# Kernel optimization log

Measured on AMD Instinct MI355X. Metric: run time of the kernel, lower is better.

## Reference

```python
import jax, jax.numpy as jnp
import numpy as np

N_NODES = 100000
N_EDGES = 1600000
IN_FEAT = 128
N_HEADS = 8
OUT_FEAT = 16


def setup_inputs() -> dict:
    key = jax.random.key(0)
    k1, k2, k3, k4, k5 = jax.random.split(key, 5)
    x = jax.random.normal(k1, (N_NODES, IN_FEAT), dtype=jnp.float32)
    edge_index = jax.random.randint(k2, (2, N_EDGES), 0, N_NODES)
    # Glorot-uniform params as in init_params
    lim_w = float(np.sqrt(6.0 / (IN_FEAT + N_HEADS * OUT_FEAT)))
    W = jax.random.uniform(k3, (IN_FEAT, N_HEADS * OUT_FEAT), minval=-lim_w, maxval=lim_w, dtype=jnp.float32)
    lim_a = float(np.sqrt(6.0 / (1 + N_HEADS * OUT_FEAT)))
    a_src = jax.random.uniform(k4, (N_HEADS, OUT_FEAT), minval=-lim_a, maxval=lim_a, dtype=jnp.float32)
    a_tgt = jax.random.uniform(k5, (N_HEADS, OUT_FEAT), minval=-lim_a, maxval=lim_a, dtype=jnp.float32)
    bias = jnp.zeros((OUT_FEAT,), dtype=jnp.float32)
    return {"in_nodes_features": x, "edge_index": edge_index, "W": W, "a_src": a_src, "a_tgt": a_tgt, "bias": bias}


def reference(in_nodes_features, edge_index, W, a_src, a_tgt, bias):
    # Single GATLayerImp3 with concat=False, activation=Softmax (GAT, num_of_layers=2).
    # Dropout disabled (eval / dropout=0.0).
    N = in_nodes_features.shape[0]
    H, F = a_src.shape
    proj = (in_nodes_features @ W).reshape(N, H, F)            # [N, H, F]
    s_src = jnp.einsum('nhf,hf->nh', proj, a_src)              # [N, H]
    s_tgt = jnp.einsum('nhf,hf->nh', proj, a_tgt)              # [N, H]
    src, tgt = edge_index[0], edge_index[1]
    # lift + per-edge LeakyReLU(0.2) scoring
    e = jax.nn.leaky_relu(s_src[src] + s_tgt[tgt], negative_slope=0.2)  # [E, H]
    # numerically stable segment softmax over edges sharing a target node
    seg_max = jax.ops.segment_max(e, tgt, num_segments=N)      # [N, H]
    seg_max = jnp.where(jnp.isfinite(seg_max), seg_max, 0.0)
    ex = jnp.exp(e - seg_max[tgt])                             # [E, H]
    denom = jax.ops.segment_sum(ex, tgt, num_segments=N)       # [N, H]
    alpha = ex / (denom[tgt] + 1e-16)                          # [E, H]
    # weighted message + scatter-add aggregation
    msg = proj[src] * alpha[:, :, None]                        # [E, H, F]
    out = jax.ops.segment_sum(msg, tgt, num_segments=N)        # [N, H, F]
    out = out.mean(axis=1) + bias                              # concat=False -> mean over heads
    return jax.nn.softmax(out, axis=-1)                        # final-layer Softmax activation
```

## Files before the change

### kernel.cpp

```cpp
#include <hip/hip_runtime.h>

#define NN 100000
#define NE 1600000

static __device__ __forceinline__ unsigned short f32_to_bf16_rne(float x) {
    unsigned int u = __float_as_uint(x);
    u += 0x7fff + ((u >> 16) & 1);
    return (unsigned short)(u >> 16);
}
static __device__ __forceinline__ float bf16_to_f32(unsigned int bits16) {
    return __uint_as_float(bits16 << 16);
}

__global__ __launch_bounds__(256) void gemm_score_kernel(const float* __restrict__ x,
                                                         const float* __restrict__ W,
                                                         const float* __restrict__ a_src,
                                                         const float* __restrict__ a_tgt,
                                                         unsigned short* __restrict__ projT,
                                                         unsigned short* __restrict__ s_src_b,
                                                         unsigned short* __restrict__ s_tgt_b) {
    __shared__ float sXT[32][68];
    __shared__ float sW[32][128];
    const int t = threadIdx.x;
    const int n0 = blockIdx.x * 64;
    const int c0 = (t & 31) * 4;
    const int r0 = t >> 5;
    float acc[8][4];
#pragma unroll
    for (int i = 0; i < 8; i++)
#pragma unroll
        for (int j = 0; j < 4; j++) acc[i][j] = 0.f;

    for (int kt = 0; kt < 128; kt += 32) {
#pragma unroll
        for (int p = 0; p < 2; p++) {
            int idx = t + p * 256;
            int r = idx >> 3;
            int kk = idx & 7;
            float4 v = make_float4(0.f, 0.f, 0.f, 0.f);
            int n = n0 + r;
            if (n < NN) v = *reinterpret_cast<const float4*>(&x[(size_t)n * 128 + kt + kk * 4]);
            sXT[kk * 4 + 0][r] = v.x;
            sXT[kk * 4 + 1][r] = v.y;
            sXT[kk * 4 + 2][r] = v.z;
            sXT[kk * 4 + 3][r] = v.w;
        }
#pragma unroll
        for (int p = 0; p < 4; p++) {
            int idx = t + p * 256;
            int kr = idx >> 5;
            int c4 = idx & 31;
            float4 v = *reinterpret_cast<const float4*>(&W[(size_t)(kt + kr) * 128 + c4 * 4]);
            *reinterpret_cast<float4*>(&sW[kr][c4 * 4]) = v;
        }
        __syncthreads();
#pragma unroll
        for (int k = 0; k < 32; k++) {
            float4 xa = *reinterpret_cast<const float4*>(&sXT[k][r0 * 8]);
            float4 xb = *reinterpret_cast<const float4*>(&sXT[k][r0 * 8 + 4]);
            float4 wv = *reinterpret_cast<const float4*>(&sW[k][c0]);
            float xs[8] = {xa.x, xa.y, xa.z, xa.w, xb.x, xb.y, xb.z, xb.w};
#pragma unroll
            for (int i = 0; i < 8; i++) {
                acc[i][0] += xs[i] * wv.x;
                acc[i][1] += xs[i] * wv.y;
                acc[i][2] += xs[i] * wv.z;
                acc[i][3] += xs[i] * wv.w;
            }
        }
        __syncthreads();
    }
    const int h  = c0 >> 4;
    const int f0 = c0 & 15;
    const float aS0 = a_src[c0], aS1 = a_src[c0 + 1], aS2 = a_src[c0 + 2], aS3 = a_src[c0 + 3];
    const float aT0 = a_tgt[c0], aT1 = a_tgt[c0 + 1], aT2 = a_tgt[c0 + 2], aT3 = a_tgt[c0 + 3];
#pragma unroll
    for (int i = 0; i < 8; i++) {
        int n = n0 + r0 * 8 + i;
        if (n < NN) {
            unsigned short* pT = &projT[(size_t)n * 128];
#pragma unroll
            for (int j = 0; j < 4; j++) pT[(f0 + j) * 8 + h] = f32_to_bf16_rne(acc[i][j]);
            float ss = acc[i][0] * aS0 + acc[i][1] * aS1 + acc[i][2] * aS2 + acc[i][3] * aS3;
            float st = acc[i][0] * aT0 + acc[i][1] * aT1 + acc[i][2] * aT2 + acc[i][3] * aT3;
            ss += __shfl_xor(ss, 1);
            ss += __shfl_xor(ss, 2);
            st += __shfl_xor(st, 1);
            st += __shfl_xor(st, 2);
            if ((t & 3) == 0) {
                s_src_b[(size_t)n * 8 + h] = f32_to_bf16_rne(ss);
                s_tgt_b[(size_t)n * 8 + h] = f32_to_bf16_rne(st);
            }
        }
    }
}

__global__ __launch_bounds__(256) void denom_kernel(const int* __restrict__ src,
                                                    const int* __restrict__ tgt,
                                                    const unsigned short* __restrict__ s_src_b,
                                                    const unsigned short* __restrict__ s_tgt_b,
                                                    float* __restrict__ denom,
                                                    unsigned short* __restrict__ exb) {
    int gid = blockIdx.x * blockDim.x + threadIdx.x;
    int e = gid >> 3;
    if (e >= NE) return;
    int h = gid & 7;
    int s = src[e], t = tgt[e];
    float v = bf16_to_f32(s_src_b[(size_t)s * 8 + h]) + bf16_to_f32(s_tgt_b[(size_t)t * 8 + h]);
    v = v >= 0.f ? v : 0.2f * v;
    float ex = expf(v);
    exb[(size_t)e * 8 + h] = f32_to_bf16_rne(ex);
    atomicAdd(&denom[(size_t)t * 8 + h], ex);
}

__global__ __launch_bounds__(256) void aggregate_kernel(const int* __restrict__ src,
                                                        const int* __restrict__ tgt,
                                                        const float* __restrict__ denom,
                                                        const unsigned short* __restrict__ exb,
                                                        const unsigned short* __restrict__ projT,
                                                        float* __restrict__ out_acc) {
    int gid = blockIdx.x * blockDim.x + threadIdx.x;
    int e = gid >> 4;
    int lane = gid & 15;
    if (e >= NE) return;
    int s = src[e], t = tgt[e];
    int h = lane & 7;
    float ex = bf16_to_f32(exb[(size_t)e * 8 + h]);
    float alpha = ex / (denom[(size_t)t * 8 + h] + 1e-16f);
    uint4 v = *reinterpret_cast<const uint4*>(&projT[(size_t)s * 128 + lane * 8]);
    float p0 = bf16_to_f32(v.x & 0xffffu), p1 = bf16_to_f32(v.x >> 16);
    float p2 = bf16_to_f32(v.y & 0xffffu), p3 = bf16_to_f32(v.y >> 16);
    float p4 = bf16_to_f32(v.z & 0xffffu), p5 = bf16_to_f32(v.z >> 16);
    float p6 = bf16_to_f32(v.w & 0xffffu), p7 = bf16_to_f32(v.w >> 16);
    float m = 0.f;
    m += __shfl(alpha, 0, 16) * p0;
    m += __shfl(alpha, 1, 16) * p1;
    m += __shfl(alpha, 2, 16) * p2;
    m += __shfl(alpha, 3, 16) * p3;
    m += __shfl(alpha, 4, 16) * p4;
    m += __shfl(alpha, 5, 16) * p5;
    m += __shfl(alpha, 6, 16) * p6;
    m += __shfl(alpha, 7, 16) * p7;
    atomicAdd(&out_acc[(size_t)t * 16 + lane], m * 0.125f);
}

__global__ __launch_bounds__(256) void softmax_kernel(const float* __restrict__ out_acc,
                                                      const float* __restrict__ bias,
                                                      float* __restrict__ out) {
    int gid = blockIdx.x * blockDim.x + threadIdx.x;
    int n = gid >> 4;
    int lane = gid & 15;
    if (n >= NN) return;
    float v = out_acc[(size_t)n * 16 + lane] + bias[lane];
    float mx = v;
#pragma unroll
    for (int m = 1; m < 16; m <<= 1) mx = fmaxf(mx, __shfl_xor(mx, m, 64));
    float ex = expf(v - mx);
    float sum = ex;
#pragma unroll
    for (int m = 1; m < 16; m <<= 1) sum += __shfl_xor(sum, m, 64);
    out[(size_t)n * 16 + lane] = ex / sum;
}

extern "C" void kernel_launch(void* const* d_in, const int* in_sizes, int n_in,
                              void* d_out, int out_size, void* d_ws, size_t ws_size,
                              hipStream_t stream) {
    const float* x     = (const float*)d_in[0];
    const int*   ei    = (const int*)d_in[1];
    const float* W     = (const float*)d_in[2];
    const float* a_src = (const float*)d_in[3];
    const float* a_tgt = (const float*)d_in[4];
    const float* bias  = (const float*)d_in[5];
    float* out = (float*)d_out;

    const int* src = ei;
    const int* tgt = ei + NE;

    char* ws = (char*)d_ws;
    size_t off = 0;
    auto alloc = [&](size_t bytes) {
        char* p = ws + off;
        off += (bytes + 255) & ~(size_t)255;
        return p;
    };
    unsigned short* projT   = (unsigned short*)alloc((size_t)NN * 128 * 2);
    unsigned short* exb     = (unsigned short*)alloc((size_t)NE * 8 * 2);
    unsigned short* s_src_b = (unsigned short*)alloc((size_t)NN * 8 * 2);
    unsigned short* s_tgt_b = (unsigned short*)alloc((size_t)NN * 8 * 2);
    float*          denom   = (float*)alloc((size_t)NN * 8 * 4);
    float*          out_acc = (float*)alloc((size_t)NN * 16 * 4);

    hipMemsetAsync(denom, 0, (size_t)NN * 8 * 4, stream);
    hipMemsetAsync(out_acc, 0, (size_t)NN * 16 * 4, stream);

    gemm_score_kernel<<<(NN + 63) / 64, 256, 0, stream>>>(x, W, a_src, a_tgt, projT, s_src_b, s_tgt_b);
    denom_kernel<<<((size_t)NE * 8 + 255) / 256, 256, 0, stream>>>(src, tgt, s_src_b, s_tgt_b, denom, exb);
    aggregate_kernel<<<((size_t)NE * 16 + 255) / 256, 256, 0, stream>>>(src, tgt, denom, exb,
                                                                        projT, out_acc);
    softmax_kernel<<<(NN * 16 + 255) / 256, 256, 0, stream>>>(out_acc, bias, out);
}
```

Measured before the change: 247.7 us.

## Recompute edge exponentials in aggregate instead of storing them; enlarge GEMM tile

The denom kernel no longer writes per-edge exp values to a bf16 buffer. The aggregate kernel recomputes them from the per-node source and target scores, which removes a 25.6 MB write and its later read in exchange for extra score gathers and exp work per edge. The projection GEMM now processes 128 nodes per block with a row-major shared tile and 16 accumulators per thread instead of 64 nodes with a transposed tile. That raises register use and changes the shared-memory access pattern.

After: 289.0 us. 1.17x slower.

```diff
diff --git a/kernel.cpp b/kernel.cpp
--- a/kernel.cpp
+++ b/kernel.cpp
@@ -19,31 +19,28 @@
                                                          unsigned short* __restrict__ projT,
                                                          unsigned short* __restrict__ s_src_b,
                                                          unsigned short* __restrict__ s_tgt_b) {
-    __shared__ float sXT[32][68];
+    __shared__ float sX[128][32];
     __shared__ float sW[32][128];
     const int t = threadIdx.x;
-    const int n0 = blockIdx.x * 64;
+    const int n0 = blockIdx.x * 128;
     const int c0 = (t & 31) * 4;
     const int r0 = t >> 5;
-    float acc[8][4];
+    float acc[16][4];
 #pragma unroll
-    for (int i = 0; i < 8; i++)
+    for (int i = 0; i < 16; i++)
 #pragma unroll
         for (int j = 0; j < 4; j++) acc[i][j] = 0.f;
 
     for (int kt = 0; kt < 128; kt += 32) {
 #pragma unroll
-        for (int p = 0; p < 2; p++) {
+        for (int p = 0; p < 4; p++) {
             int idx = t + p * 256;
             int r = idx >> 3;
             int kk = idx & 7;
             float4 v = make_float4(0.f, 0.f, 0.f, 0.f);
             int n = n0 + r;
             if (n < NN) v = *reinterpret_cast<const float4*>(&x[(size_t)n * 128 + kt + kk * 4]);
-            sXT[kk * 4 + 0][r] = v.x;
-            sXT[kk * 4 + 1][r] = v.y;
-            sXT[kk * 4 + 2][r] = v.z;
-            sXT[kk * 4 + 3][r] = v.w;
+            *reinterpret_cast<float4*>(&sX[r][kk * 4]) = v;
         }
 #pragma unroll
         for (int p = 0; p < 4; p++) {
@@ -56,16 +53,14 @@
         __syncthreads();
 #pragma unroll
         for (int k = 0; k < 32; k++) {
-            float4 xa = *reinterpret_cast<const float4*>(&sXT[k][r0 * 8]);
-            float4 xb = *reinterpret_cast<const float4*>(&sXT[k][r0 * 8 + 4]);
             float4 wv = *reinterpret_cast<const float4*>(&sW[k][c0]);
-            float xs[8] = {xa.x, xa.y, xa.z, xa.w, xb.x, xb.y, xb.z, xb.w};
 #pragma unroll
-            for (int i = 0; i < 8; i++) {
-                acc[i][0] += xs[i] * wv.x;
-                acc[i][1] += xs[i] * wv.y;
-                acc[i][2] += xs[i] * wv.z;
-                acc[i][3] += xs[i] * wv.w;
+            for (int i = 0; i < 16; i++) {
+                float xv = sX[r0 + 8 * i][k];
+                acc[i][0] += xv * wv.x;
+                acc[i][1] += xv * wv.y;
+                acc[i][2] += xv * wv.z;
+                acc[i][3] += xv * wv.w;
             }
         }
         __syncthreads();
@@ -75,8 +70,8 @@
     const float aS0 = a_src[c0], aS1 = a_src[c0 + 1], aS2 = a_src[c0 + 2], aS3 = a_src[c0 + 3];
     const float aT0 = a_tgt[c0], aT1 = a_tgt[c0 + 1], aT2 = a_tgt[c0 + 2], aT3 = a_tgt[c0 + 3];
 #pragma unroll
-    for (int i = 0; i < 8; i++) {
-        int n = n0 + r0 * 8 + i;
+    for (int i = 0; i < 16; i++) {
+        int n = n0 + r0 + 8 * i;
         if (n < NN) {
             unsigned short* pT = &projT[(size_t)n * 128];
 #pragma unroll
@@ -99,8 +94,7 @@
                                                     const int* __restrict__ tgt,
                                                     const unsigned short* __restrict__ s_src_b,
                                                     const unsigned short* __restrict__ s_tgt_b,
-                                                    float* __restrict__ denom,
-                                                    unsigned short* __restrict__ exb) {
+                                                    float* __restrict__ denom) {
     int gid = blockIdx.x * blockDim.x + threadIdx.x;
     int e = gid >> 3;
     if (e >= NE) return;
@@ -108,15 +102,14 @@
     int s = src[e], t = tgt[e];
     float v = bf16_to_f32(s_src_b[(size_t)s * 8 + h]) + bf16_to_f32(s_tgt_b[(size_t)t * 8 + h]);
     v = v >= 0.f ? v : 0.2f * v;
-    float ex = expf(v);
-    exb[(size_t)e * 8 + h] = f32_to_bf16_rne(ex);
-    atomicAdd(&denom[(size_t)t * 8 + h], ex);
+    atomicAdd(&denom[(size_t)t * 8 + h], expf(v));
 }
 
 __global__ __launch_bounds__(256) void aggregate_kernel(const int* __restrict__ src,
                                                         const int* __restrict__ tgt,
+                                                        const unsigned short* __restrict__ s_src_b,
+                                                        const unsigned short* __restrict__ s_tgt_b,
                                                         const float* __restrict__ denom,
-                                                        const unsigned short* __restrict__ exb,
                                                         const unsigned short* __restrict__ projT,
                                                         float* __restrict__ out_acc) {
     int gid = blockIdx.x * blockDim.x + threadIdx.x;
@@ -125,7 +118,9 @@
     if (e >= NE) return;
     int s = src[e], t = tgt[e];
     int h = lane & 7;
-    float ex = bf16_to_f32(exb[(size_t)e * 8 + h]);
+    float v0 = bf16_to_f32(s_src_b[(size_t)s * 8 + h]) + bf16_to_f32(s_tgt_b[(size_t)t * 8 + h]);
+    v0 = v0 >= 0.f ? v0 : 0.2f * v0;
+    float ex = expf(v0);
     float alpha = ex / (denom[(size_t)t * 8 + h] + 1e-16f);
     uint4 v = *reinterpret_cast<const uint4*>(&projT[(size_t)s * 128 + lane * 8]);
     float p0 = bf16_to_f32(v.x & 0xffffu), p1 = bf16_to_f32(v.x >> 16);
@@ -184,7 +179,6 @@
         return p;
     };
     unsigned short* projT   = (unsigned short*)alloc((size_t)NN * 128 * 2);
-    unsigned short* exb     = (unsigned short*)alloc((size_t)NE * 8 * 2);
     unsigned short* s_src_b = (unsigned short*)alloc((size_t)NN * 8 * 2);
     unsigned short* s_tgt_b = (unsigned short*)alloc((size_t)NN * 8 * 2);
     float*          denom   = (float*)alloc((size_t)NN * 8 * 4);
@@ -193,9 +187,9 @@
     hipMemsetAsync(denom, 0, (size_t)NN * 8 * 4, stream);
     hipMemsetAsync(out_acc, 0, (size_t)NN * 16 * 4, stream);
 
-    gemm_score_kernel<<<(NN + 63) / 64, 256, 0, stream>>>(x, W, a_src, a_tgt, projT, s_src_b, s_tgt_b);
-    denom_kernel<<<((size_t)NE * 8 + 255) / 256, 256, 0, stream>>>(src, tgt, s_src_b, s_tgt_b, denom, exb);
-    aggregate_kernel<<<((size_t)NE * 16 + 255) / 256, 256, 0, stream>>>(src, tgt, denom, exb,
-                                                                        projT, out_acc);
+    gemm_score_kernel<<<(NN + 127) / 128, 256, 0, stream>>>(x, W, a_src, a_tgt, projT, s_src_b, s_tgt_b);
+    denom_kernel<<<((size_t)NE * 8 + 255) / 256, 256, 0, stream>>>(src, tgt, s_src_b, s_tgt_b, denom);
+    aggregate_kernel<<<((size_t)NE * 16 + 255) / 256, 256, 0, stream>>>(src, tgt, s_src_b, s_tgt_b,
+                                                                        denom, projT, out_acc);
     softmax_kernel<<<(NN * 16 + 255) / 256, 256, 0, stream>>>(out_acc, bias, out);
 }
```

## Bucket edges by target block and fuse softmax-aggregate into per-bucket kernel

Applied to the files above, without the earlier changes.

Edges are counting-sorted into buckets of 128 target nodes, using a histogram, a scan and a scatter that packs src and local target into one int. A single fused kernel per bucket then computes the edge softmax denominators, the weighted aggregation and the final softmax in shared memory. This replaces global atomics, the exb buffer and two memsets. It adds three sorting kernels and shared-memory atomics, and the fused kernel may suffer from uneven bucket sizes and only 782 blocks.

New measurement: 440.6 us. 1.78x slower.

```diff
diff --git a/kernel.cpp b/kernel.cpp
--- a/kernel.cpp
+++ b/kernel.cpp
@@ -2,6 +2,7 @@
 
 #define NN 100000
 #define NE 1600000
+#define NBUCK 782
 
 static __device__ __forceinline__ unsigned short f32_to_bf16_rne(float x) {
     unsigned int u = __float_as_uint(x);
@@ -95,71 +96,146 @@
     }
 }
 
-__global__ __launch_bounds__(256) void denom_kernel(const int* __restrict__ src,
-                                                    const int* __restrict__ tgt,
-                                                    const unsigned short* __restrict__ s_src_b,
-                                                    const unsigned short* __restrict__ s_tgt_b,
-                                                    float* __restrict__ denom,
-                                                    unsigned short* __restrict__ exb) {
-    int gid = blockIdx.x * blockDim.x + threadIdx.x;
-    int e = gid >> 3;
-    if (e >= NE) return;
-    int h = gid & 7;
-    int s = src[e], t = tgt[e];
-    float v = bf16_to_f32(s_src_b[(size_t)s * 8 + h]) + bf16_to_f32(s_tgt_b[(size_t)t * 8 + h]);
-    v = v >= 0.f ? v : 0.2f * v;
-    float ex = expf(v);
-    exb[(size_t)e * 8 + h] = f32_to_bf16_rne(ex);
-    atomicAdd(&denom[(size_t)t * 8 + h], ex);
-}
-
-__global__ __launch_bounds__(256) void aggregate_kernel(const int* __restrict__ src,
-                                                        const int* __restrict__ tgt,
-                                                        const float* __restrict__ denom,
-                                                        const unsigned short* __restrict__ exb,
-                                                        const unsigned short* __restrict__ projT,
-                                                        float* __restrict__ out_acc) {
-    int gid = blockIdx.x * blockDim.x + threadIdx.x;
-    int e = gid >> 4;
-    int lane = gid & 15;
-    if (e >= NE) return;
-    int s = src[e], t = tgt[e];
-    int h = lane & 7;
-    float ex = bf16_to_f32(exb[(size_t)e * 8 + h]);
-    float alpha = ex / (denom[(size_t)t * 8 + h] + 1e-16f);
-    uint4 v = *reinterpret_cast<const uint4*>(&projT[(size_t)s * 128 + lane * 8]);
-    float p0 = bf16_to_f32(v.x & 0xffffu), p1 = bf16_to_f32(v.x >> 16);
-    float p2 = bf16_to_f32(v.y & 0xffffu), p3 = bf16_to_f32(v.y >> 16);
-    float p4 = bf16_to_f32(v.z & 0xffffu), p5 = bf16_to_f32(v.z >> 16);
-    float p6 = bf16_to_f32(v.w & 0xffffu), p7 = bf16_to_f32(v.w >> 16);
-    float m = 0.f;
-    m += __shfl(alpha, 0, 16) * p0;
-    m += __shfl(alpha, 1, 16) * p1;
-    m += __shfl(alpha, 2, 16) * p2;
-    m += __shfl(alpha, 3, 16) * p3;
-    m += __shfl(alpha, 4, 16) * p4;
-    m += __shfl(alpha, 5, 16) * p5;
-    m += __shfl(alpha, 6, 16) * p6;
-    m += __shfl(alpha, 7, 16) * p7;
-    atomicAdd(&out_acc[(size_t)t * 16 + lane], m * 0.125f);
-}
-
-__global__ __launch_bounds__(256) void softmax_kernel(const float* __restrict__ out_acc,
-                                                      const float* __restrict__ bias,
-                                                      float* __restrict__ out) {
-    int gid = blockIdx.x * blockDim.x + threadIdx.x;
-    int n = gid >> 4;
-    int lane = gid & 15;
-    if (n >= NN) return;
-    float v = out_acc[(size_t)n * 16 + lane] + bias[lane];
-    float mx = v;
-#pragma unroll
-    for (int m = 1; m < 16; m <<= 1) mx = fmaxf(mx, __shfl_xor(mx, m, 64));
-    float ex = expf(v - mx);
-    float sum = ex;
-#pragma unroll
-    for (int m = 1; m < 16; m <<= 1) sum += __shfl_xor(sum, m, 64);
-    out[(size_t)n * 16 + lane] = ex / sum;
+__global__ __launch_bounds__(256) void bucket_hist_kernel(const int* __restrict__ tgt,
+                                                          int* __restrict__ counts) {
+    __shared__ int bins[NBUCK];
+    for (int i = threadIdx.x; i < NBUCK; i += 256) bins[i] = 0;
+    __syncthreads();
+    int base = blockIdx.x * 2048;
+#pragma unroll
+    for (int i = 0; i < 8; i++) {
+        int e = base + i * 256 + threadIdx.x;
+        if (e < NE) atomicAdd(&bins[tgt[e] >> 7], 1);
+    }
+    __syncthreads();
+    for (int i = threadIdx.x; i < NBUCK; i += 256)
+        if (bins[i]) atomicAdd(&counts[i], bins[i]);
+}
+
+__global__ __launch_bounds__(1024) void bucket_scan_kernel(const int* __restrict__ counts,
+                                                           int* __restrict__ base,
+                                                           int* __restrict__ gcursor) {
+    __shared__ int sc[1024];
+    int t = threadIdx.x;
+    int v = (t < NBUCK) ? counts[t] : 0;
+    sc[t] = v;
+    __syncthreads();
+    for (int off = 1; off < 1024; off <<= 1) {
+        int u = (t >= off) ? sc[t - off] : 0;
+        __syncthreads();
+        sc[t] += u;
+        __syncthreads();
+    }
+    if (t < NBUCK) {
+        int ex = sc[t] - v;
+        base[t] = ex;
+        gcursor[t] = ex;
+    }
+    if (t == NBUCK - 1) base[NBUCK] = sc[t];
+}
+
+__global__ __launch_bounds__(256) void bucket_scatter_kernel(const int* __restrict__ src,
+                                                             const int* __restrict__ tgt,
+                                                             int* __restrict__ gcursor,
+                                                             int* __restrict__ sorted) {
+    __shared__ int bins[NBUCK];
+    __shared__ int basel[NBUCK];
+    for (int i = threadIdx.x; i < NBUCK; i += 256) bins[i] = 0;
+    __syncthreads();
+    int blk = blockIdx.x * 2048;
+    int myb[8], myr[8], myp[8];
+#pragma unroll
+    for (int i = 0; i < 8; i++) {
+        int e = blk + i * 256 + threadIdx.x;
+        if (e < NE) {
+            int tg = tgt[e];
+            int b = tg >> 7;
+            myb[i] = b;
+            myr[i] = atomicAdd(&bins[b], 1);
+            myp[i] = (src[e] << 7) | (tg & 127);
+        } else myb[i] = -1;
+    }
+    __syncthreads();
+    for (int i = threadIdx.x; i < NBUCK; i += 256) {
+        int c = bins[i];
+        basel[i] = c ? atomicAdd(&gcursor[i], c) : 0;
+    }
+    __syncthreads();
+#pragma unroll
+    for (int i = 0; i < 8; i++)
+        if (myb[i] >= 0) sorted[basel[myb[i]] + myr[i]] = myp[i];
+}
+
+__global__ __launch_bounds__(256) void fused_bucket_kernel(const int* __restrict__ base,
+                                                           const int* __restrict__ sorted,
+                                                           const unsigned short* __restrict__ s_src_b,
+                                                           const unsigned short* __restrict__ s_tgt_b,
+                                                           const unsigned short* __restrict__ projT,
+                                                           const float* __restrict__ bias,
+                                                           float* __restrict__ out) {
+    __shared__ unsigned short stl[128 * 8];
+    __shared__ float dnl[128 * 8];
+    __shared__ float outl[128 * 16];
+    const int t = threadIdx.x;
+    const int node0 = blockIdx.x * 128;
+    for (int i = t; i < 1024; i += 256) {
+        int node = node0 + (i >> 3);
+        stl[i] = (node < NN) ? s_tgt_b[(size_t)node * 8 + (i & 7)] : (unsigned short)0;
+        dnl[i] = 0.f;
+    }
+    for (int i = t; i < 2048; i += 256) outl[i] = 0.f;
+    __syncthreads();
+    const int e0 = base[blockIdx.x], e1 = base[blockIdx.x + 1];
+    const int ne = e1 - e0;
+
+    for (int idx = t; idx < ne * 8; idx += 256) {
+        int e = e0 + (idx >> 3), h = idx & 7;
+        int p = sorted[e];
+        int s = p >> 7, loc = p & 127;
+        float v = bf16_to_f32(s_src_b[(size_t)s * 8 + h]) + bf16_to_f32(stl[loc * 8 + h]);
+        v = v >= 0.f ? v : 0.2f * v;
+        atomicAdd(&dnl[loc * 8 + h], expf(v));
+    }
+    __syncthreads();
+
+    for (int idx = t; idx < ne * 16; idx += 256) {
+        int e = e0 + (idx >> 4), f = idx & 15, h = f & 7;
+        int p = sorted[e];
+        int s = p >> 7, loc = p & 127;
+        float v0 = bf16_to_f32(s_src_b[(size_t)s * 8 + h]) + bf16_to_f32(stl[loc * 8 + h]);
+        v0 = v0 >= 0.f ? v0 : 0.2f * v0;
+        float alpha = expf(v0) / (dnl[loc * 8 + h] + 1e-16f);
+        uint4 v = *reinterpret_cast<const uint4*>(&projT[(size_t)s * 128 + f * 8]);
+        float p0 = bf16_to_f32(v.x & 0xffffu), p1 = bf16_to_f32(v.x >> 16);
+        float p2 = bf16_to_f32(v.y & 0xffffu), p3 = bf16_to_f32(v.y >> 16);
+        float p4 = bf16_to_f32(v.z & 0xffffu), p5 = bf16_to_f32(v.z >> 16);
+        float p6 = bf16_to_f32(v.w & 0xffffu), p7 = bf16_to_f32(v.w >> 16);
+        float m = 0.f;
+        m += __shfl(alpha, 0, 16) * p0;
+        m += __shfl(alpha, 1, 16) * p1;
+        m += __shfl(alpha, 2, 16) * p2;
+        m += __shfl(alpha, 3, 16) * p3;
+        m += __shfl(alpha, 4, 16) * p4;
+        m += __shfl(alpha, 5, 16) * p5;
+        m += __shfl(alpha, 6, 16) * p6;
+        m += __shfl(alpha, 7, 16) * p7;
+        atomicAdd(&outl[loc * 16 + f], m * 0.125f);
+    }
+    __syncthreads();
+
+    for (int idx = t; idx < 2048; idx += 256) {
+        int loc = idx >> 4, f = idx & 15;
+        int node = node0 + loc;
+        float v = outl[idx] + bias[f];
+        float mx = v;
+#pragma unroll
+        for (int mm = 1; mm < 16; mm <<= 1) mx = fmaxf(mx, __shfl_xor(mx, mm, 16));
+        float ex = expf(v - mx);
+        float sum = ex;
+#pragma unroll
+        for (int mm = 1; mm < 16; mm <<= 1) sum += __shfl_xor(sum, mm, 16);
+        if (node < NN) out[(size_t)node * 16 + f] = ex / sum;
+    }
 }
 
 extern "C" void kernel_launch(void* const* d_in, const int* in_sizes, int n_in,
@@ -184,18 +260,18 @@
         return p;
     };
     unsigned short* projT   = (unsigned short*)alloc((size_t)NN * 128 * 2);
-    unsigned short* exb     = (unsigned short*)alloc((size_t)NE * 8 * 2);
     unsigned short* s_src_b = (unsigned short*)alloc((size_t)NN * 8 * 2);
     unsigned short* s_tgt_b = (unsigned short*)alloc((size_t)NN * 8 * 2);
-    float*          denom   = (float*)alloc((size_t)NN * 8 * 4);
-    float*          out_acc = (float*)alloc((size_t)NN * 16 * 4);
-
-    hipMemsetAsync(denom, 0, (size_t)NN * 8 * 4, stream);
-    hipMemsetAsync(out_acc, 0, (size_t)NN * 16 * 4, stream);
+    int*            counts  = (int*)alloc((size_t)NBUCK * 4);
+    int*            bbase   = (int*)alloc((size_t)(NBUCK + 1) * 4);
+    int*            gcursor = (int*)alloc((size_t)NBUCK * 4);
+    int*            sorted  = (int*)alloc((size_t)NE * 4);
+
+    hipMemsetAsync(counts, 0, (size_t)NBUCK * 4, stream);
 
     gemm_score_kernel<<<(NN + 63) / 64, 256, 0, stream>>>(x, W, a_src, a_tgt, projT, s_src_b, s_tgt_b);
-    denom_kernel<<<((size_t)NE * 8 + 255) / 256, 256, 0, stream>>>(src, tgt, s_src_b, s_tgt_b, denom, exb);
-    aggregate_kernel<<<((size_t)NE * 16 + 255) / 256, 256, 0, stream>>>(src, tgt, denom, exb,
-                                                                        projT, out_acc);
-    softmax_kernel<<<(NN * 16 + 255) / 256, 256, 0, stream>>>(out_acc, bias, out);
-}
+    bucket_hist_kernel<<<(NE + 2047) / 2048, 256, 0, stream>>>(tgt, counts);
+    bucket_scan_kernel<<<1, 1024, 0, stream>>>(counts, bbase, gcursor);
+    bucket_scatter_kernel<<<(NE + 2047) / 2048, 256, 0, stream>>>(src, tgt, gcursor, sorted);
+    fused_bucket_kernel<<<NBUCK, 256, 0, stream>>>(bbase, sorted, s_src_b, s_tgt_b, projT, bias, out);
+}
```

## Bucket-sort edges by source node block to localize projT gathers

Applied to the files above, without the earlier changes.

Adds a three-kernel counting sort (histogram, scan, scatter) that groups edges into buckets of 1024 source nodes, packing (src,tgt) pairs into an int2 array. The denom and aggregate kernels then walk edges in this order, so projT and s_src gathers hit a small, cache-resident window of source rows instead of random rows. The cost is an extra pass over the edge list, a 12.8MB write and read of the sorted pairs, and three extra launches. The target-side atomics stay random.

Result: slower. 293.0 us (+18.3%).

```diff
diff --git a/kernel.cpp b/kernel.cpp
--- a/kernel.cpp
+++ b/kernel.cpp
@@ -2,6 +2,7 @@
 
 #define NN 100000
 #define NE 1600000
+#define NBUCK 98
 
 static __device__ __forceinline__ unsigned short f32_to_bf16_rne(float x) {
     unsigned int u = __float_as_uint(x);
@@ -95,8 +96,72 @@
     }
 }
 
-__global__ __launch_bounds__(256) void denom_kernel(const int* __restrict__ src,
-                                                    const int* __restrict__ tgt,
+__global__ __launch_bounds__(256) void bucket_hist_kernel(const int* __restrict__ src,
+                                                          int* __restrict__ counts) {
+    __shared__ int bins[NBUCK];
+    for (int i = threadIdx.x; i < NBUCK; i += 256) bins[i] = 0;
+    __syncthreads();
+    int base = blockIdx.x * 2048;
+#pragma unroll
+    for (int i = 0; i < 8; i++) {
+        int e = base + i * 256 + threadIdx.x;
+        if (e < NE) atomicAdd(&bins[src[e] >> 10], 1);
+    }
+    __syncthreads();
+    for (int i = threadIdx.x; i < NBUCK; i += 256)
+        if (bins[i]) atomicAdd(&counts[i], bins[i]);
+}
+
+__global__ __launch_bounds__(128) void bucket_scan_kernel(const int* __restrict__ counts,
+                                                          int* __restrict__ gcursor) {
+    __shared__ int sc[128];
+    int t = threadIdx.x;
+    int v = (t < NBUCK) ? counts[t] : 0;
+    sc[t] = v;
+    __syncthreads();
+    for (int off = 1; off < 128; off <<= 1) {
+        int u = (t >= off) ? sc[t - off] : 0;
+        __syncthreads();
+        sc[t] += u;
+        __syncthreads();
+    }
+    if (t < NBUCK) gcursor[t] = sc[t] - v;
+}
+
+__global__ __launch_bounds__(256) void bucket_scatter_kernel(const int* __restrict__ src,
+                                                             const int* __restrict__ tgt,
+                                                             int* __restrict__ gcursor,
+                                                             int2* __restrict__ sorted) {
+    __shared__ int bins[NBUCK];
+    __shared__ int basel[NBUCK];
+    for (int i = threadIdx.x; i < NBUCK; i += 256) bins[i] = 0;
+    __syncthreads();
+    int blk = blockIdx.x * 2048;
+    int myb[8], myr[8];
+    int2 myp[8];
+#pragma unroll
+    for (int i = 0; i < 8; i++) {
+        int e = blk + i * 256 + threadIdx.x;
+        if (e < NE) {
+            int s = src[e];
+            int b = s >> 10;
+            myb[i] = b;
+            myr[i] = atomicAdd(&bins[b], 1);
+            myp[i] = make_int2(s, tgt[e]);
+        } else myb[i] = -1;
+    }
+    __syncthreads();
+    for (int i = threadIdx.x; i < NBUCK; i += 256) {
+        int c = bins[i];
+        basel[i] = c ? atomicAdd(&gcursor[i], c) : 0;
+    }
+    __syncthreads();
+#pragma unroll
+    for (int i = 0; i < 8; i++)
+        if (myb[i] >= 0) sorted[basel[myb[i]] + myr[i]] = myp[i];
+}
+
+__global__ __launch_bounds__(256) void denom_kernel(const int2* __restrict__ sorted,
                                                     const unsigned short* __restrict__ s_src_b,
                                                     const unsigned short* __restrict__ s_tgt_b,
                                                     float* __restrict__ denom,
@@ -105,16 +170,15 @@
     int e = gid >> 3;
     if (e >= NE) return;
     int h = gid & 7;
-    int s = src[e], t = tgt[e];
-    float v = bf16_to_f32(s_src_b[(size_t)s * 8 + h]) + bf16_to_f32(s_tgt_b[(size_t)t * 8 + h]);
+    int2 p = sorted[e];
+    float v = bf16_to_f32(s_src_b[(size_t)p.x * 8 + h]) + bf16_to_f32(s_tgt_b[(size_t)p.y * 8 + h]);
     v = v >= 0.f ? v : 0.2f * v;
     float ex = expf(v);
     exb[(size_t)e * 8 + h] = f32_to_bf16_rne(ex);
-    atomicAdd(&denom[(size_t)t * 8 + h], ex);
-}
-
-__global__ __launch_bounds__(256) void aggregate_kernel(const int* __restrict__ src,
-                                                        const int* __restrict__ tgt,
+    atomicAdd(&denom[(size_t)p.y * 8 + h], ex);
+}
+
+__global__ __launch_bounds__(256) void aggregate_kernel(const int2* __restrict__ sorted,
                                                         const float* __restrict__ denom,
                                                         const unsigned short* __restrict__ exb,
                                                         const unsigned short* __restrict__ projT,
@@ -123,11 +187,11 @@
     int e = gid >> 4;
     int lane = gid & 15;
     if (e >= NE) return;
-    int s = src[e], t = tgt[e];
+    int2 p = sorted[e];
     int h = lane & 7;
     float ex = bf16_to_f32(exb[(size_t)e * 8 + h]);
-    float alpha = ex / (denom[(size_t)t * 8 + h] + 1e-16f);
-    uint4 v = *reinterpret_cast<const uint4*>(&projT[(size_t)s * 128 + lane * 8]);
+    float alpha = ex / (denom[(size_t)p.y * 8 + h] + 1e-16f);
+    uint4 v = *reinterpret_cast<const uint4*>(&projT[(size_t)p.x * 128 + lane * 8]);
     float p0 = bf16_to_f32(v.x & 0xffffu), p1 = bf16_to_f32(v.x >> 16);
     float p2 = bf16_to_f32(v.y & 0xffffu), p3 = bf16_to_f32(v.y >> 16);
     float p4 = bf16_to_f32(v.z & 0xffffu), p5 = bf16_to_f32(v.z >> 16);
@@ -141,7 +205,7 @@
     m += __shfl(alpha, 5, 16) * p5;
     m += __shfl(alpha, 6, 16) * p6;
     m += __shfl(alpha, 7, 16) * p7;
-    atomicAdd(&out_acc[(size_t)t * 16 + lane], m * 0.125f);
+    atomicAdd(&out_acc[(size_t)p.y * 16 + lane], m * 0.125f);
 }
 
 __global__ __launch_bounds__(256) void softmax_kernel(const float* __restrict__ out_acc,
@@ -189,13 +253,20 @@
     unsigned short* s_tgt_b = (unsigned short*)alloc((size_t)NN * 8 * 2);
     float*          denom   = (float*)alloc((size_t)NN * 8 * 4);
     float*          out_acc = (float*)alloc((size_t)NN * 16 * 4);
-
+    int*            counts  = (int*)alloc((size_t)NBUCK * 4);
+    int*            gcursor = (int*)alloc((size_t)NBUCK * 4);
+    int2*           sorted  = (int2*)alloc((size_t)NE * 8);
+
+    hipMemsetAsync(counts, 0, (size_t)NBUCK * 4, stream);
     hipMemsetAsync(denom, 0, (size_t)NN * 8 * 4, stream);
     hipMemsetAsync(out_acc, 0, (size_t)NN * 16 * 4, stream);
 
     gemm_score_kernel<<<(NN + 63) / 64, 256, 0, stream>>>(x, W, a_src, a_tgt, projT, s_src_b, s_tgt_b);
-    denom_kernel<<<((size_t)NE * 8 + 255) / 256, 256, 0, stream>>>(src, tgt, s_src_b, s_tgt_b, denom, exb);
-    aggregate_kernel<<<((size_t)NE * 16 + 255) / 256, 256, 0, stream>>>(src, tgt, denom, exb,
+    bucket_hist_kernel<<<(NE + 2047) / 2048, 256, 0, stream>>>(src, counts);
+    bucket_scan_kernel<<<1, 128, 0, stream>>>(counts, gcursor);
+    bucket_scatter_kernel<<<(NE + 2047) / 2048, 256, 0, stream>>>(src, tgt, gcursor, sorted);
+    denom_kernel<<<((size_t)NE * 8 + 255) / 256, 256, 0, stream>>>(sorted, s_src_b, s_tgt_b, denom, exb);
+    aggregate_kernel<<<((size_t)NE * 16 + 255) / 256, 256, 0, stream>>>(sorted, denom, exb,
                                                                         projT, out_acc);
     softmax_kernel<<<(NN * 16 + 255) / 256, 256, 0, stream>>>(out_acc, bias, out);
 }
```
